# Optimization experiments

Measured on AMD Instinct MI355X. Metric: run time of the kernel, lower is better.

Reference implementation:

```python
import jax, jax.numpy as jnp
import numpy as np

B, NA, NB, E = 2, 256, 256, 512
H1, H2 = 300, 100


def setup_inputs() -> dict:
    key = jax.random.key(0)
    ks = jax.random.split(key, 16)

    def n(k, shape, scale=1.0):
        return jax.random.normal(k, shape, dtype=jnp.float32) * scale

    z = lambda shape: jnp.zeros(shape, jnp.float32)
    return {
        "action_embedding": n(ks[0], (B, E, NA)),
        "anchor_embedding": n(ks[1], (B, E, NB)),
        "action_points": n(ks[2], (B, 3, NA)),
        "anchor_points": n(ks[3], (B, 3, NB)),
        # pairwise MLP kernel params: 2E -> 300 -> 100 -> 1
        "mlp_W1": n(ks[4], (2 * E, H1), (2 * E) ** -0.5),
        "mlp_b1": z((H1,)),
        "mlp_W2": n(ks[5], (H1, H2), H1 ** -0.5),
        "mlp_b2": z((H2,)),
        "mlp_W3": n(ks[6], (H2, 1), H2 ** -0.5),
        "mlp_b3": z((1,)),
        # PointNet [512,64,64,64,128,512] (1x1 convs) + Conv1d(512,1,bias=False)
        "pn_W0": n(ks[7], (64, 512), 512 ** -0.5),
        "pn_b0": z((64,)),
        "pn_W1": n(ks[8], (64, 64), 64 ** -0.5),
        "pn_b1": z((64,)),
        "pn_W2": n(ks[9], (64, 64), 64 ** -0.5),
        "pn_b2": z((64,)),
        "pn_W3": n(ks[10], (128, 64), 64 ** -0.5),
        "pn_b3": z((128,)),
        "pn_W4": n(ks[11], (512, 128), 128 ** -0.5),
        "pn_b4": z((512,)),
        "head_W": n(ks[12], (1, 512), 512 ** -0.5),
    }


def reference(action_embedding, anchor_embedding, action_points, anchor_points,
              mlp_W1, mlp_b1, mlp_W2, mlp_b2, mlp_W3, mlp_b3,
              pn_W0, pn_b0, pn_W1, pn_b1, pn_W2, pn_b2, pn_W3, pn_b3,
              pn_W4, pn_b4, head_W):
    P_A = action_points.transpose(0, 2, 1)      # (B, NA, 3)
    P_B = anchor_points.transpose(0, 2, 1)      # (B, NB, 3)
    Phi_A = action_embedding.transpose(0, 2, 1)  # (B, NA, E)
    Phi_B = anchor_embedding.transpose(0, 2, 1)  # (B, NB, E)
    Ed = Phi_A.shape[-1]

    # --- symmetric pairwise MLP kernel: softplus((mlp(cat(a,b)) + mlp(cat(b,a))) / 2) ---
    # First Linear layer is split so the O(NA*NB*2E) concat is never materialized:
    # cat(a,b) @ W1 == a @ W1[:E] + b @ W1[E:]
    W1a, W1b = mlp_W1[:Ed], mlp_W1[Ed:]

    def mlp_tail(h):  # h: (B, NA, NB, H1) pre-activation of layer 1
        h = jax.nn.relu(h)
        h = jax.nn.relu(h @ mlp_W2 + mlp_b2)
        return (h @ mlp_W3 + mlp_b3)[..., 0]  # (B, NA, NB)

    hA_a = Phi_A @ W1a  # (B, NA, H1)
    hA_b = Phi_A @ W1b
    hB_a = Phi_B @ W1a  # (B, NB, H1)
    hB_b = Phi_B @ W1b
    v1 = mlp_tail(hA_a[:, :, None, :] + hB_b[:, None, :, :] + mlp_b1)  # mlp(cat(x1,x2))
    v2 = mlp_tail(hB_a[:, None, :, :] + hA_b[:, :, None, :] + mlp_b1)  # mlp(cat(x2,x1))
    R_est = jax.nn.softplus((v1 + v2) * 0.5)  # (B, NA, NB) estimated distances

    # --- weighted multilateration (estimate_p), vectorized over (B, NA) ---
    # Linearized LS: ||p||^2 - 2 q_k^T p = r_k^2 - ||q_k||^2; subtract weighted means
    # to eliminate ||p||^2, then solve 3x3 weighted normal equations per action point.
    w = jnp.ones(P_B.shape[:2], R_est.dtype)            # (B, NB) uniform weights (last_attn=False)
    wsum = w.sum(-1, keepdims=True)                      # (B, 1)
    qbar = (w[..., None] * P_B).sum(1) / wsum            # (B, 3)
    bvec = (P_B ** 2).sum(-1)[:, None, :] - R_est ** 2   # (B, NA, NB)
    bbar = (w[:, None, :] * bvec).sum(-1) / wsum         # (B, NA)
    Amat = 2.0 * (P_B - qbar[:, None, :])                # (B, NB, 3)
    yvec = bvec - bbar[..., None]                        # (B, NA, NB)
    M = jnp.einsum('bki,bk,bkj->bij', Amat, w, Amat)     # (B, 3, 3)
    rhs = jnp.einsum('bki,bk,bak->bai', Amat, w, yvec)   # (B, NA, 3)
    P_A_B_pred = jnp.linalg.solve(M[:, None], rhs[..., None])[..., 0]  # (B, NA, 3)

    flow = (P_A_B_pred - P_A).transpose(0, 2, 1)         # (B, 3, NA)

    # --- PointNet flow-weight head (1x1 convs + ReLU, final conv no bias) ---
    x = action_embedding                                  # (B, 512, NA)
    for Wc, bc in ((pn_W0, pn_b0), (pn_W1, pn_b1), (pn_W2, pn_b2),
                   (pn_W3, pn_b3), (pn_W4, pn_b4)):
        x = jax.nn.relu(jnp.einsum('oi,bin->bon', Wc, x) + bc[None, :, None])
    weight = jnp.einsum('oi,bin->bon', head_W, x)        # (B, 1, NA)

    full_flow = jnp.concatenate([flow, weight], axis=1)  # (B, 4, NA)
    return full_flow
```

## Files before the change

### kernel.cpp

```cpp
#include <hip/hip_runtime.h>
#include <hip/hip_bf16.h>
#include <hip/hip_fp16.h>

typedef float f32x4 __attribute__((ext_vector_type(4)));
typedef float f32x16 __attribute__((ext_vector_type(16)));
typedef short s16x8 __attribute__((ext_vector_type(8)));
typedef _Float16 f16x8 __attribute__((ext_vector_type(8)));

#define OFF_EMBT   0u
#define OFF_W1T    1048576u
#define OFF_W2TSW  1662976u
#define OFF_W0BF   1740800u
#define OFF_HA     1806336u
#define OFF_R2     3051520u
#define WS_TOTAL   3575808u

__device__ __forceinline__ int pack_bf2(float a, float b) {
  __hip_bfloat162 h = __float22bfloat162_rn(make_float2(a, b));
  int r; __builtin_memcpy(&r, &h, 4); return r;
}
__device__ __forceinline__ unsigned pack_f16_2(float a, float b) {
  __half2 h = __float22half2_rn(make_float2(a, b));
  unsigned r; __builtin_memcpy(&r, &h, 4); return r;
}
__device__ __forceinline__ unsigned short bf16u(float f) {
  __hip_bfloat16 h = __float2bfloat16(f);
  unsigned short u; __builtin_memcpy(&u, &h, 2); return u;
}
__device__ __forceinline__ s16x8 i4_to_s8(int a, int b, int c, int d) {
  union { int i[4]; s16x8 s; } u;
  u.i[0] = a; u.i[1] = b; u.i[2] = c; u.i[3] = d; return u.s;
}
template<int CTRL>
__device__ __forceinline__ float dpp_add(float x) {
  int xi; __builtin_memcpy(&xi, &x, 4);
  int yi = __builtin_amdgcn_update_dpp(0, xi, CTRL, 0xf, 0xf, true);
  float y; __builtin_memcpy(&y, &yi, 4);
  return x + y;
}
__device__ __forceinline__ float swz_xor16(float x) {
  int xi; __builtin_memcpy(&xi, &x, 4);
  int yi = __builtin_amdgcn_ds_swizzle(xi, 0x401f);
  float y; __builtin_memcpy(&y, &yi, 4);
  return y;
}

__global__ __launch_bounds__(256) void ka_prep(
    const float* __restrict__ act_emb, const float* __restrict__ anc_emb,
    const float* __restrict__ W1, const float* __restrict__ W2,
    const float* __restrict__ W0pn, char* __restrict__ ws)
{
  __hip_bfloat16* embT  = (__hip_bfloat16*)(ws + OFF_EMBT);
  __hip_bfloat16* W1T   = (__hip_bfloat16*)(ws + OFF_W1T);
  unsigned short* W2Tsw = (unsigned short*)(ws + OFF_W2TSW);
  unsigned short* W0bf  = (unsigned short*)(ws + OFF_W0BF);
  __shared__ float tile[64][65];
  int blk = blockIdx.x, t = threadIdx.x;
  if (blk < 128) {
    int b = blk >> 6, emb = (blk >> 5) & 1, ntile = (blk >> 3) & 3, etile = blk & 7;
    const float* src = emb ? anc_emb : act_emb;
    int e0 = etile * 64, n0 = ntile * 64;
    int rr = t >> 6, cc = t & 63;
    #pragma unroll
    for (int it2 = 0; it2 < 16; ++it2) {
      int e_l = rr * 16 + it2;
      tile[e_l][cc] = src[(size_t)(b * 512 + e0 + e_l) * 256 + n0 + cc];
    }
    __syncthreads();
    int n_l = t >> 2, eq = t & 3;
    unsigned int* dst = (unsigned int*)(embT + ((size_t)((b * 2 + emb) * 256 + n0 + n_l)) * 512 + e0 + eq * 16);
    #pragma unroll
    for (int kk = 0; kk < 8; ++kk)
      dst[kk] = (unsigned)pack_bf2(tile[eq * 16 + 2 * kk][n_l], tile[eq * 16 + 2 * kk + 1][n_l]);
  } else if (blk < 208) {
    int id = blk - 128;
    int half = id / 40; int rem = id % 40; int et = rem / 5; int ct = rem % 5;
    int e0 = et * 64, c0 = ct * 64;
    int rr = t >> 6, cc = t & 63;
    #pragma unroll
    for (int it2 = 0; it2 < 16; ++it2) {
      int e_l = rr * 16 + it2;
      int c = c0 + cc;
      tile[e_l][cc] = (c < 300) ? W1[(size_t)(half * 512 + e0 + e_l) * 300 + c] : 0.f;
    }
    __syncthreads();
    int c_l = t >> 2, eq = t & 3;
    if (c0 + c_l < 300) {
      unsigned int* dst = (unsigned int*)(W1T + ((size_t)(half * 300 + c0 + c_l)) * 512 + e0 + eq * 16);
      #pragma unroll
      for (int kk = 0; kk < 8; ++kk)
        dst[kk] = (unsigned)pack_bf2(tile[eq * 16 + 2 * kk][c_l], tile[eq * 16 + 2 * kk + 1][c_l]);
    }
  } else if (blk < 227) {
    int idx = (blk - 208) * 256 + t;
    int lane = idx & 63; int ntks = idx >> 6; int nt = ntks & 3; int ks = ntks >> 2;
    int n = nt * 32 + (lane & 31);
    int kb = ks * 16 + (lane >> 5) * 8;
    unsigned int q[4];
    #pragma unroll
    for (int jj = 0; jj < 4; ++jj) {
      int k0 = kb + jj * 2, k1 = kb + jj * 2 + 1;
      float f0 = (n < 100 && k0 < 300) ? W2[(size_t)k0 * 100 + n] : 0.f;
      float f1 = (n < 100 && k1 < 300) ? W2[(size_t)k1 * 100 + n] : 0.f;
      q[jj] = pack_f16_2(f0, f1);
    }
    ((uint4*)W2Tsw)[idx] = make_uint4(q[0], q[1], q[2], q[3]);
  } else if (blk < 243) {
    int idx = (blk - 227) * 256 + t;
    const float* s = W0pn + (size_t)idx * 8;
    ((uint4*)W0bf)[idx] = make_uint4(
        (unsigned)pack_bf2(s[0], s[1]), (unsigned)pack_bf2(s[2], s[3]),
        (unsigned)pack_bf2(s[4], s[5]), (unsigned)pack_bf2(s[6], s[7]));
  } else {
    int idx = (blk - 243) * 256 + t;
    _Float16* haf = (_Float16*)(ws + OFF_HA);
    #pragma unroll
    for (int u2 = 0; u2 < 2; ++u2) {
      int unit = idx * 2 + u2;
      int combo = unit >> 5, row = unit & 31;
      size_t off = (((size_t)combo * 19 + 18) << 9) + (1 << 8) + (row << 3) + 4;
      unsigned* p = (unsigned*)(haf + off);
      p[0] = 0u; p[1] = 0u;
    }
  }
}

template<int K, int NT>
__device__ __forceinline__ void pn_layer(unsigned short* xb, const float* __restrict__ W,
                                         const float* __restrict__ bias, int wv, int l, int g)
{
  constexpr int NN = NT / 4;
  f32x4 z = {0.f, 0.f, 0.f, 0.f};
  f32x4 acc[NN];
  #pragma unroll
  for (int nn = 0; nn < NN; ++nn) acc[nn] = z;
  #pragma unroll
  for (int nn = 0; nn < NN; ++nn) {
    int o = (wv + nn * 4) * 16 + l;
    const float* wr0 = W + (size_t)o * K;
    #pragma unroll
    for (int ks = 0; ks < K / 32; ++ks) {
      int koff = ks * 32 + g * 8;
      f32x4 wa = *(const f32x4*)(wr0 + koff);
      f32x4 wb = *(const f32x4*)(wr0 + koff + 4);
      s16x8 bfr = i4_to_s8(pack_bf2(wa.x, wa.y), pack_bf2(wa.z, wa.w),
                           pack_bf2(wb.x, wb.y), pack_bf2(wb.z, wb.w));
      s16x8 a0 = *(const s16x8*)(xb + (size_t)l * 520 + koff);
      acc[nn] = __builtin_amdgcn_mfma_f32_16x16x32_bf16(a0, bfr, acc[nn], 0, 0, 0);
    }
  }
  __syncthreads();
  #pragma unroll
  for (int nn = 0; nn < NN; ++nn) {
    int chan = (wv + nn * 4) * 16 + l;
    float bv = bias[chan];
    #pragma unroll
    for (int r = 0; r < 4; ++r)
      xb[(size_t)(g * 4 + r) * 520 + chan] = bf16u(fmaxf(acc[nn][r] + bv, 0.f));
  }
  __syncthreads();
}

__global__ __launch_bounds__(256) void k1_ha(
    const __hip_bfloat16* __restrict__ embT, const __hip_bfloat16* __restrict__ W1T,
    const float* __restrict__ b1, _Float16* __restrict__ ha_f,
    const unsigned short* __restrict__ W0bf,
    const float* __restrict__ pnW1, const float* __restrict__ pnW2,
    const float* __restrict__ pnW3, const float* __restrict__ pnW4,
    const float* __restrict__ pnB0, const float* __restrict__ pnB1,
    const float* __restrict__ pnB2, const float* __restrict__ pnB3,
    const float* __restrict__ pnB4,
    const float* __restrict__ headW, float* __restrict__ out)
{
  __shared__ unsigned short xbuf[16 * 520];
  int blk = blockIdx.x, t = threadIdx.x;
  int wv = t >> 6, lane = t & 63, l = lane & 15, g = lane >> 4;
  if (blk < 320) {
    int b = blk / 160; int r = blk % 160; int emb = r / 80; r %= 80;
    int mch = r / 5; int nch = r % 5;
    int m0 = mch * 16;
    const unsigned short* Ap = (const unsigned short*)embT +
        ((size_t)((b * 2 + emb) * 256 + m0 + l)) * 512;
    const unsigned short* Wp = (const unsigned short*)W1T;
    f32x4 z = {0.f, 0.f, 0.f, 0.f};
    f32x4 acc[2] = {z, z};
    for (int ks = 0; ks < 16; ++ks) {
      int k0 = ks * 32 + g * 8;
      s16x8 af = *(const s16x8*)(Ap + k0);
      #pragma unroll
      for (int q = 0; q < 2; ++q) {
        int c = nch * 120 + (wv * 2 + q) * 16 + l;
        s16x8 bf = {0, 0, 0, 0, 0, 0, 0, 0};
        if (c < 600) bf = *(const s16x8*)(Wp + (size_t)c * 512 + k0);
        acc[q] = __builtin_amdgcn_mfma_f32_16x16x32_bf16(af, bf, acc[q], 0, 0, 0);
      }
    }
    #pragma unroll
    for (int q = 0; q < 2; ++q) {
      int cl = (wv * 2 + q) * 16 + l;
      int c = nch * 120 + cl;
      if (cl < 120 && c < 600) {
        int half = (c >= 300) ? 1 : 0;
        int cc = c - half * 300;
        float bias = (emb == 0) ? b1[cc] : 0.f;
        int d = emb * 2 + half;
        int ksf = cc >> 4, hi2 = (cc >> 3) & 1, e = cc & 7;
        #pragma unroll
        for (int r2 = 0; r2 < 4; ++r2) {
          int i = m0 + g * 4 + r2;
          size_t off = (((((size_t)(b * 4 + d)) * 8 + (i >> 5)) * 19 + ksf) << 9)
                     + (hi2 << 8) + ((i & 31) << 3) + e;
          ha_f[off] = (_Float16)__float2half_rn(acc[q][r2] + bias);
        }
      }
    }
  } else {
    int pn = blk - 320;
    int b_pn = pn >> 4, n0 = (pn & 15) * 16;
    unsigned short* xb = xbuf;
    {
      const unsigned short* A0 = (const unsigned short*)embT + ((size_t)(b_pn * 2 * 256 + n0)) * 512;
      f32x4 acc0 = {0.f, 0.f, 0.f, 0.f};
      int o = wv * 16 + l;
      const unsigned short* w0r = W0bf + (size_t)o * 512;
      #pragma unroll
      for (int ks = 0; ks < 16; ++ks) {
        int koff = ks * 32 + g * 8;
        s16x8 bfr = *(const s16x8*)(w0r + koff);
        s16x8 a0 = *(const s16x8*)(A0 + (size_t)l * 512 + koff);
        acc0 = __builtin_amdgcn_mfma_f32_16x16x32_bf16(a0, bfr, acc0, 0, 0, 0);
      }
      float bv = pnB0[o];
      #pragma unroll
      for (int r2 = 0; r2 < 4; ++r2)
        xb[(size_t)(g * 4 + r2) * 520 + o] = bf16u(fmaxf(acc0[r2] + bv, 0.f));
      __syncthreads();
    }
    pn_layer<64, 4>(xb, pnW1, pnB1, wv, l, g);
    pn_layer<64, 4>(xb, pnW2, pnB2, wv, l, g);
    pn_layer<64, 8>(xb, pnW3, pnB3, wv, l, g);
    pn_layer<128, 32>(xb, pnW4, pnB4, wv, l, g);
    {
      int p_l = t >> 4, os = t & 15;
      const unsigned short* row = xb + (size_t)p_l * 520 + os * 32;
      float s = 0.f;
      #pragma unroll
      for (int c = 0; c < 32; ++c) {
        unsigned int u = ((unsigned int)row[c]) << 16;
        float xv; __builtin_memcpy(&xv, &u, 4);
        s += xv * headW[os * 32 + c];
      }
      s += __shfl_xor(s, 1); s += __shfl_xor(s, 2);
      s += __shfl_xor(s, 4); s += __shfl_xor(s, 8);
      if (os == 0) out[(size_t)(b_pn * 4 + 3) * 256 + n0 + p_l] = s;
    }
  }
}

__global__ __launch_bounds__(512, 2) void k2_main(
    const _Float16* __restrict__ haF, const unsigned short* __restrict__ W2Tsw,
    const float* __restrict__ b2g, const float* __restrict__ W3g, const float* __restrict__ b3g,
    float* __restrict__ R2)
{
  __shared__ int4 w2s[4864];
  int blkp = blockIdx.x, t = threadIdx.x;
  int blk = (blkp & 7) * 64 + (blkp >> 3);
  int wv = t >> 6, lane = t & 63, col = lane & 31, hi = lane >> 5;
  int u = blk; int b = u >> 8; u &= 255; int it = u >> 5; int jtp = u & 31;
  int i0 = it * 32;
  int j = jtp * 8 + wv;
  {
    const int4* w2g = (const int4*)W2Tsw;
    #pragma unroll
    for (int q = 0; q < 9; ++q) { int idx = t + q * 512; w2s[idx] = w2g[idx]; }
    { int idx = t + 9 * 512; if (idx < 4864) w2s[idx] = w2g[idx]; }
  }
  const _Float16* pA0 = haF + ((((size_t)(b * 4 + 0)) * 8 + it) * 19) * 512 + lane * 8;
  const _Float16* pA1 = haF + ((((size_t)(b * 4 + 1)) * 8 + it) * 19) * 512 + lane * 8;
  const _Float16* pB0 = haF + ((((size_t)(b * 4 + 3)) * 8 + (j >> 5)) * 19) * 512
                        + (hi * 32 + (j & 31)) * 8;
  const _Float16* pB1 = haF + ((((size_t)(b * 4 + 2)) * 8 + (j >> 5)) * 19) * 512
                        + (hi * 32 + (j & 31)) * 8;
  f16x8 a0c = *(const f16x8*)(pA0);
  f16x8 a1c = *(const f16x8*)(pA1);
  f16x8 b0c = *(const f16x8*)(pB0);
  f16x8 b1c = *(const f16x8*)(pB1);
  __syncthreads();

  const f16x8 zf = {0, 0, 0, 0, 0, 0, 0, 0};
  f32x16 z16;
  #pragma unroll
  for (int q = 0; q < 16; ++q) z16[q] = 0.f;
  f32x16 acc00 = z16, acc01 = z16, acc02 = z16, acc03 = z16;
  f32x16 acc10 = z16, acc11 = z16, acc12 = z16, acc13 = z16;

  #pragma unroll 1
  for (int ks = 0; ks < 19; ++ks) {
    f16x8 a0n, a1n, b0n, b1n;
    if (ks < 18) {
      int ko = (ks + 1) * 512;
      a0n = *(const f16x8*)(pA0 + ko);
      a1n = *(const f16x8*)(pA1 + ko);
      b0n = *(const f16x8*)(pB0 + ko);
      b1n = *(const f16x8*)(pB1 + ko);
    } else { a0n = a0c; a1n = a1c; b0n = b0c; b1n = b1c; }
    f16x8 af0 = __builtin_elementwise_max(a0c + b0c, zf);
    f16x8 af1 = __builtin_elementwise_max(a1c + b1c, zf);
    const int4* wp = &w2s[ks * 256 + lane];
    f16x8 bf0 = *(const f16x8*)(wp);
    f16x8 bf1 = *(const f16x8*)(wp + 64);
    f16x8 bf2 = *(const f16x8*)(wp + 128);
    f16x8 bf3 = *(const f16x8*)(wp + 192);
    acc00 = __builtin_amdgcn_mfma_f32_32x32x16_f16(af0, bf0, acc00, 0, 0, 0);
    acc10 = __builtin_amdgcn_mfma_f32_32x32x16_f16(af1, bf0, acc10, 0, 0, 0);
    acc01 = __builtin_amdgcn_mfma_f32_32x32x16_f16(af0, bf1, acc01, 0, 0, 0);
    acc11 = __builtin_amdgcn_mfma_f32_32x32x16_f16(af1, bf1, acc11, 0, 0, 0);
    acc02 = __builtin_amdgcn_mfma_f32_32x32x16_f16(af0, bf2, acc02, 0, 0, 0);
    acc12 = __builtin_amdgcn_mfma_f32_32x32x16_f16(af1, bf2, acc12, 0, 0, 0);
    acc03 = __builtin_amdgcn_mfma_f32_32x32x16_f16(af0, bf3, acc03, 0, 0, 0);
    acc13 = __builtin_amdgcn_mfma_f32_32x32x16_f16(af1, bf3, acc13, 0, 0, 0);
    a0c = a0n; a1c = a1n; b0c = b0n; b1c = b1n;
  }
  {
    float w3v[4], b2v[4];
    #pragma unroll
    for (int nt = 0; nt < 4; ++nt) {
      int n = nt * 32 + col;
      w3v[nt] = (n < 100) ? W3g[n] : 0.f;
      b2v[nt] = (n < 100) ? b2g[n] : 0.f;
    }
    float b3 = b3g[0];
    float mine = 0.f;
    #pragma unroll
    for (int r = 0; r < 16; ++r) {
      float x = fmaxf(acc00[r] + b2v[0], 0.f) * w3v[0] + fmaxf(acc10[r] + b2v[0], 0.f) * w3v[0]
              + fmaxf(acc01[r] + b2v[1], 0.f) * w3v[1] + fmaxf(acc11[r] + b2v[1], 0.f) * w3v[1]
              + fmaxf(acc02[r] + b2v[2], 0.f) * w3v[2] + fmaxf(acc12[r] + b2v[2], 0.f) * w3v[2]
              + fmaxf(acc03[r] + b2v[3], 0.f) * w3v[3] + fmaxf(acc13[r] + b2v[3], 0.f) * w3v[3];
      x = dpp_add<0xB1>(x);
      x = dpp_add<0x4E>(x);
      x = dpp_add<0x141>(x);
      x = dpp_add<0x140>(x);
      x += swz_xor16(x);
      if (col == r) mine = x;
    }
    if (col < 16) {
      float S = 0.5f * mine + b3;
      float Rr = (S > 20.f) ? S : log1pf(expf(S));
      int il = (col & 3) + 8 * (col >> 2) + 4 * hi;
      R2[((size_t)(b * 256 + i0 + il)) * 256 + j] = Rr * Rr;
    }
  }
}

__device__ __forceinline__ float block_sum(float v, float* redbuf, int t) {
  #pragma unroll
  for (int m = 1; m < 64; m <<= 1) v += __shfl_xor(v, m);
  __syncthreads();
  if ((t & 63) == 0) redbuf[t >> 6] = v;
  __syncthreads();
  return redbuf[0] + redbuf[1] + redbuf[2] + redbuf[3];
}

__global__ __launch_bounds__(256) void k3_solve(
    const float* __restrict__ anc_pts, const float* __restrict__ act_pts,
    const float* __restrict__ R2, float* __restrict__ out)
{
  __shared__ float Ax[256], Ay[256], Az[256];
  __shared__ float redbuf[4];
  int blk = blockIdx.x, t = threadIdx.x;
  int b = blk >> 2, ic = blk & 3;
  int k = t;
  float px = anc_pts[(size_t)(b * 3 + 0) * 256 + k];
  float py = anc_pts[(size_t)(b * 3 + 1) * 256 + k];
  float pz = anc_pts[(size_t)(b * 3 + 2) * 256 + k];
  float qx = block_sum(px, redbuf, t) * (1.f / 256.f);
  float qy = block_sum(py, redbuf, t) * (1.f / 256.f);
  float qz = block_sum(pz, redbuf, t) * (1.f / 256.f);
  float ax = 2.f * (px - qx), ay = 2.f * (py - qy), az = 2.f * (pz - qz);
  float p2 = px * px + py * py + pz * pz;
  Ax[k] = ax; Ay[k] = ay; Az[k] = az;
  float mxx = block_sum(ax * ax, redbuf, t);
  float mxy = block_sum(ax * ay, redbuf, t);
  float mxz = block_sum(ax * az, redbuf, t);
  float myy = block_sum(ay * ay, redbuf, t);
  float myz = block_sum(ay * az, redbuf, t);
  float mzz = block_sum(az * az, redbuf, t);
  float c0x = block_sum(ax * p2, redbuf, t);
  float c0y = block_sum(ay * p2, redbuf, t);
  float c0z = block_sum(az * p2, redbuf, t);
  __syncthreads();
  float det = mxx * (myy * mzz - myz * myz) - mxy * (mxy * mzz - myz * mxz) + mxz * (mxy * myz - myy * mxz);
  float idet = 1.f / det;
  float i00 = (myy * mzz - myz * myz) * idet;
  float i01 = (mxz * myz - mxy * mzz) * idet;
  float i02 = (mxy * myz - mxz * myy) * idet;
  float i11 = (mxx * mzz - mxz * mxz) * idet;
  float i12 = (mxy * mxz - mxx * myz) * idet;
  float i22 = (mxx * myy - mxy * mxy) * idet;
  int il = t >> 2, ks = t & 3;
  int i = ic * 64 + il;
  const float* rrow = R2 + ((size_t)(b * 256 + i)) * 256;
  float r0 = 0.f, r1 = 0.f, r2 = 0.f;
  #pragma unroll
  for (int kk = 0; kk < 16; ++kk) {
    int kb = ks * 64 + kk * 4;
    f32x4 rv = *(const f32x4*)(rrow + kb);
    r0 += Ax[kb] * rv.x + Ax[kb + 1] * rv.y + Ax[kb + 2] * rv.z + Ax[kb + 3] * rv.w;
    r1 += Ay[kb] * rv.x + Ay[kb + 1] * rv.y + Ay[kb + 2] * rv.z + Ay[kb + 3] * rv.w;
    r2 += Az[kb] * rv.x + Az[kb + 1] * rv.y + Az[kb + 2] * rv.z + Az[kb + 3] * rv.w;
  }
  r0 += __shfl_xor(r0, 1); r0 += __shfl_xor(r0, 2);
  r1 += __shfl_xor(r1, 1); r1 += __shfl_xor(r1, 2);
  r2 += __shfl_xor(r2, 1); r2 += __shfl_xor(r2, 2);
  if (ks == 0) {
    float hx = c0x - r0, hy = c0y - r1, hz = c0z - r2;
    float x0 = i00 * hx + i01 * hy + i02 * hz;
    float x1 = i01 * hx + i11 * hy + i12 * hz;
    float x2 = i02 * hx + i12 * hy + i22 * hz;
    out[(size_t)(b * 4 + 0) * 256 + i] = x0 - act_pts[(size_t)(b * 3 + 0) * 256 + i];
    out[(size_t)(b * 4 + 1) * 256 + i] = x1 - act_pts[(size_t)(b * 3 + 1) * 256 + i];
    out[(size_t)(b * 4 + 2) * 256 + i] = x2 - act_pts[(size_t)(b * 3 + 2) * 256 + i];
  }
}

extern "C" void kernel_launch(void* const* d_in, const int* in_sizes, int n_in,
                              void* d_out, int out_size, void* d_ws, size_t ws_size,
                              hipStream_t stream)
{
  const float* act_emb = (const float*)d_in[0];
  const float* anc_emb = (const float*)d_in[1];
  const float* act_pts = (const float*)d_in[2];
  const float* anc_pts = (const float*)d_in[3];
  const float* W1  = (const float*)d_in[4];
  const float* b1  = (const float*)d_in[5];
  const float* W2  = (const float*)d_in[6];
  const float* b2  = (const float*)d_in[7];
  const float* W3  = (const float*)d_in[8];
  const float* b3  = (const float*)d_in[9];
  const float* pnW0 = (const float*)d_in[10];
  const float* pnB0 = (const float*)d_in[11];
  const float* pnW1 = (const float*)d_in[12];
  const float* pnB1 = (const float*)d_in[13];
  const float* pnW2 = (const float*)d_in[14];
  const float* pnB2 = (const float*)d_in[15];
  const float* pnW3 = (const float*)d_in[16];
  const float* pnB3 = (const float*)d_in[17];
  const float* pnW4 = (const float*)d_in[18];
  const float* pnB4 = (const float*)d_in[19];
  const float* headW = (const float*)d_in[20];
  char* ws = (char*)d_ws;
  __hip_bfloat16* embT  = (__hip_bfloat16*)(ws + OFF_EMBT);
  __hip_bfloat16* W1T   = (__hip_bfloat16*)(ws + OFF_W1T);
  unsigned short* W2Tsw = (unsigned short*)(ws + OFF_W2TSW);
  unsigned short* W0bf  = (unsigned short*)(ws + OFF_W0BF);
  _Float16* ha_f = (_Float16*)(ws + OFF_HA);
  float* R2ws  = (float*)(ws + OFF_R2);
  float* outp  = (float*)d_out;

  ka_prep<<<247, 256, 0, stream>>>(act_emb, anc_emb, W1, W2, pnW0, ws);
  k1_ha<<<352, 256, 0, stream>>>(embT, W1T, b1, ha_f, W0bf,
                                 pnW1, pnW2, pnW3, pnW4, pnB0, pnB1, pnB2, pnB3, pnB4,
                                 headW, outp);
  k2_main<<<512, 512, 0, stream>>>(ha_f, W2Tsw, b2, W3, b3, R2ws);
  k3_solve<<<8, 256, 0, stream>>>(anc_pts, act_pts, R2ws, outp);
}
```

Baseline: 155.2 us.

## Pre-pack PointNet weights to bf16, retile pairwise MLP waves, widen solve grid

PointNet layer weights 1-4 are now converted to bf16 once in the prep kernel, so the per-block fp32 loads and repacking in k1 go away. In k2 each wave now covers two j columns and half of the output-channel tiles instead of one column and all four. This halves the LDS weight-fragment reads per MFMA and loads adjacent B rows together. The two wave halves combine partial sums through a small shared buffer, which adds two barriers. k3_solve launches 16 blocks instead of 8, with each block handling 32 rows, to spread the tail reduction over more CUs.

```diff
diff --git a/kernel.cpp b/kernel.cpp
--- a/kernel.cpp
+++ b/kernel.cpp
@@ -13,7 +13,8 @@
 #define OFF_W0BF   1740800u
 #define OFF_HA     1806336u
 #define OFF_R2     3051520u
-#define WS_TOTAL   3575808u
+#define OFF_PNPK   3575808u
+#define WS_TOTAL   3739648u
 
 __device__ __forceinline__ int pack_bf2(float a, float b) {
   __hip_bfloat162 h = __float22bfloat162_rn(make_float2(a, b));
@@ -26,10 +27,6 @@
 __device__ __forceinline__ unsigned short bf16u(float f) {
   __hip_bfloat16 h = __float2bfloat16(f);
   unsigned short u; __builtin_memcpy(&u, &h, 2); return u;
-}
-__device__ __forceinline__ s16x8 i4_to_s8(int a, int b, int c, int d) {
-  union { int i[4]; s16x8 s; } u;
-  u.i[0] = a; u.i[1] = b; u.i[2] = c; u.i[3] = d; return u.s;
 }
 template<int CTRL>
 __device__ __forceinline__ float dpp_add(float x) {
@@ -48,7 +45,10 @@
 __global__ __launch_bounds__(256) void ka_prep(
     const float* __restrict__ act_emb, const float* __restrict__ anc_emb,
     const float* __restrict__ W1, const float* __restrict__ W2,
-    const float* __restrict__ W0pn, char* __restrict__ ws)
+    const float* __restrict__ W0pn,
+    const float* __restrict__ pnW1, const float* __restrict__ pnW2,
+    const float* __restrict__ pnW3, const float* __restrict__ pnW4,
+    char* __restrict__ ws)
 {
   __hip_bfloat16* embT  = (__hip_bfloat16*)(ws + OFF_EMBT);
   __hip_bfloat16* W1T   = (__hip_bfloat16*)(ws + OFF_W1T);
@@ -111,7 +111,7 @@
     ((uint4*)W0bf)[idx] = make_uint4(
         (unsigned)pack_bf2(s[0], s[1]), (unsigned)pack_bf2(s[2], s[3]),
         (unsigned)pack_bf2(s[4], s[5]), (unsigned)pack_bf2(s[6], s[7]));
-  } else {
+  } else if (blk < 247) {
     int idx = (blk - 243) * 256 + t;
     _Float16* haf = (_Float16*)(ws + OFF_HA);
     #pragma unroll
@@ -122,11 +122,22 @@
       unsigned* p = (unsigned*)(haf + off);
       p[0] = 0u; p[1] = 0u;
     }
+  } else {
+    int idx = (blk - 247) * 256 + t;
+    const float* s;
+    if (idx < 512)       s = pnW1 + (size_t)idx * 8;
+    else if (idx < 1024) s = pnW2 + (size_t)(idx - 512) * 8;
+    else if (idx < 2048) s = pnW3 + (size_t)(idx - 1024) * 8;
+    else                 s = pnW4 + (size_t)(idx - 2048) * 8;
+    unsigned short* pnPK = (unsigned short*)(ws + OFF_PNPK);
+    ((uint4*)pnPK)[idx] = make_uint4(
+        (unsigned)pack_bf2(s[0], s[1]), (unsigned)pack_bf2(s[2], s[3]),
+        (unsigned)pack_bf2(s[4], s[5]), (unsigned)pack_bf2(s[6], s[7]));
   }
 }
 
 template<int K, int NT>
-__device__ __forceinline__ void pn_layer(unsigned short* xb, const float* __restrict__ W,
+__device__ __forceinline__ void pn_layer(unsigned short* xb, const unsigned short* __restrict__ Wp,
                                          const float* __restrict__ bias, int wv, int l, int g)
 {
   constexpr int NN = NT / 4;
@@ -137,14 +148,11 @@
   #pragma unroll
   for (int nn = 0; nn < NN; ++nn) {
     int o = (wv + nn * 4) * 16 + l;
-    const float* wr0 = W + (size_t)o * K;
+    const unsigned short* wr0 = Wp + (size_t)o * K;
     #pragma unroll
     for (int ks = 0; ks < K / 32; ++ks) {
       int koff = ks * 32 + g * 8;
-      f32x4 wa = *(const f32x4*)(wr0 + koff);
-      f32x4 wb = *(const f32x4*)(wr0 + koff + 4);
-      s16x8 bfr = i4_to_s8(pack_bf2(wa.x, wa.y), pack_bf2(wa.z, wa.w),
-                           pack_bf2(wb.x, wb.y), pack_bf2(wb.z, wb.w));
+      s16x8 bfr = *(const s16x8*)(wr0 + koff);
       s16x8 a0 = *(const s16x8*)(xb + (size_t)l * 520 + koff);
       acc[nn] = __builtin_amdgcn_mfma_f32_16x16x32_bf16(a0, bfr, acc[nn], 0, 0, 0);
     }
@@ -164,9 +172,7 @@
 __global__ __launch_bounds__(256) void k1_ha(
     const __hip_bfloat16* __restrict__ embT, const __hip_bfloat16* __restrict__ W1T,
     const float* __restrict__ b1, _Float16* __restrict__ ha_f,
-    const unsigned short* __restrict__ W0bf,
-    const float* __restrict__ pnW1, const float* __restrict__ pnW2,
-    const float* __restrict__ pnW3, const float* __restrict__ pnW4,
+    const unsigned short* __restrict__ W0bf, const unsigned short* __restrict__ pnPK,
     const float* __restrict__ pnB0, const float* __restrict__ pnB1,
     const float* __restrict__ pnB2, const float* __restrict__ pnB3,
     const float* __restrict__ pnB4,
@@ -236,10 +242,10 @@
         xb[(size_t)(g * 4 + r2) * 520 + o] = bf16u(fmaxf(acc0[r2] + bv, 0.f));
       __syncthreads();
     }
-    pn_layer<64, 4>(xb, pnW1, pnB1, wv, l, g);
-    pn_layer<64, 4>(xb, pnW2, pnB2, wv, l, g);
-    pn_layer<64, 8>(xb, pnW3, pnB3, wv, l, g);
-    pn_layer<128, 32>(xb, pnW4, pnB4, wv, l, g);
+    pn_layer<64, 4>(xb, pnPK, pnB1, wv, l, g);
+    pn_layer<64, 4>(xb, pnPK + 4096, pnB2, wv, l, g);
+    pn_layer<64, 8>(xb, pnPK + 8192, pnB3, wv, l, g);
+    pn_layer<128, 32>(xb, pnPK + 16384, pnB4, wv, l, g);
     {
       int p_l = t >> 4, os = t & 15;
       const unsigned short* row = xb + (size_t)p_l * 520 + os * 32;
@@ -263,12 +269,14 @@
     float* __restrict__ R2)
 {
   __shared__ int4 w2s[4864];
+  __shared__ float ex[4][2][2][16];
   int blkp = blockIdx.x, t = threadIdx.x;
   int blk = (blkp & 7) * 64 + (blkp >> 3);
   int wv = t >> 6, lane = t & 63, col = lane & 31, hi = lane >> 5;
+  int jl = wv & 3, nh = wv >> 2;
   int u = blk; int b = u >> 8; u &= 255; int it = u >> 5; int jtp = u & 31;
   int i0 = it * 32;
-  int j = jtp * 8 + wv;
+  int j0 = jtp * 8 + jl * 2;
   {
     const int4* w2g = (const int4*)W2Tsw;
     #pragma unroll
@@ -277,78 +285,91 @@
   }
   const _Float16* pA0 = haF + ((((size_t)(b * 4 + 0)) * 8 + it) * 19) * 512 + lane * 8;
   const _Float16* pA1 = haF + ((((size_t)(b * 4 + 1)) * 8 + it) * 19) * 512 + lane * 8;
-  const _Float16* pB0 = haF + ((((size_t)(b * 4 + 3)) * 8 + (j >> 5)) * 19) * 512
-                        + (hi * 32 + (j & 31)) * 8;
-  const _Float16* pB1 = haF + ((((size_t)(b * 4 + 2)) * 8 + (j >> 5)) * 19) * 512
-                        + (hi * 32 + (j & 31)) * 8;
+  const _Float16* pB00 = haF + ((((size_t)(b * 4 + 3)) * 8 + (j0 >> 5)) * 19) * 512
+                         + (hi * 32 + (j0 & 31)) * 8;
+  const _Float16* pB10 = haF + ((((size_t)(b * 4 + 2)) * 8 + (j0 >> 5)) * 19) * 512
+                         + (hi * 32 + (j0 & 31)) * 8;
   f16x8 a0c = *(const f16x8*)(pA0);
   f16x8 a1c = *(const f16x8*)(pA1);
-  f16x8 b0c = *(const f16x8*)(pB0);
-  f16x8 b1c = *(const f16x8*)(pB1);
+  f16x8 b00c = *(const f16x8*)(pB00);
+  f16x8 b01c = *(const f16x8*)(pB00 + 8);
+  f16x8 b10c = *(const f16x8*)(pB10);
+  f16x8 b11c = *(const f16x8*)(pB10 + 8);
   __syncthreads();
 
   const f16x8 zf = {0, 0, 0, 0, 0, 0, 0, 0};
   f32x16 z16;
   #pragma unroll
   for (int q = 0; q < 16; ++q) z16[q] = 0.f;
-  f32x16 acc00 = z16, acc01 = z16, acc02 = z16, acc03 = z16;
-  f32x16 acc10 = z16, acc11 = z16, acc12 = z16, acc13 = z16;
+  f32x16 aJ0D0N0 = z16, aJ0D0N1 = z16, aJ0D1N0 = z16, aJ0D1N1 = z16;
+  f32x16 aJ1D0N0 = z16, aJ1D0N1 = z16, aJ1D1N0 = z16, aJ1D1N1 = z16;
 
   #pragma unroll 1
   for (int ks = 0; ks < 19; ++ks) {
-    f16x8 a0n, a1n, b0n, b1n;
+    f16x8 a0n, a1n, b00n, b01n, b10n, b11n;
     if (ks < 18) {
       int ko = (ks + 1) * 512;
       a0n = *(const f16x8*)(pA0 + ko);
       a1n = *(const f16x8*)(pA1 + ko);
-      b0n = *(const f16x8*)(pB0 + ko);
-      b1n = *(const f16x8*)(pB1 + ko);
-    } else { a0n = a0c; a1n = a1c; b0n = b0c; b1n = b1c; }
-    f16x8 af0 = __builtin_elementwise_max(a0c + b0c, zf);
-    f16x8 af1 = __builtin_elementwise_max(a1c + b1c, zf);
-    const int4* wp = &w2s[ks * 256 + lane];
-    f16x8 bf0 = *(const f16x8*)(wp);
-    f16x8 bf1 = *(const f16x8*)(wp + 64);
-    f16x8 bf2 = *(const f16x8*)(wp + 128);
-    f16x8 bf3 = *(const f16x8*)(wp + 192);
-    acc00 = __builtin_amdgcn_mfma_f32_32x32x16_f16(af0, bf0, acc00, 0, 0, 0);
-    acc10 = __builtin_amdgcn_mfma_f32_32x32x16_f16(af1, bf0, acc10, 0, 0, 0);
-    acc01 = __builtin_amdgcn_mfma_f32_32x32x16_f16(af0, bf1, acc01, 0, 0, 0);
-    acc11 = __builtin_amdgcn_mfma_f32_32x32x16_f16(af1, bf1, acc11, 0, 0, 0);
-    acc02 = __builtin_amdgcn_mfma_f32_32x32x16_f16(af0, bf2, acc02, 0, 0, 0);
-    acc12 = __builtin_amdgcn_mfma_f32_32x32x16_f16(af1, bf2, acc12, 0, 0, 0);
-    acc03 = __builtin_amdgcn_mfma_f32_32x32x16_f16(af0, bf3, acc03, 0, 0, 0);
-    acc13 = __builtin_amdgcn_mfma_f32_32x32x16_f16(af1, bf3, acc13, 0, 0, 0);
-    a0c = a0n; a1c = a1n; b0c = b0n; b1c = b1n;
+      b00n = *(const f16x8*)(pB00 + ko);
+      b01n = *(const f16x8*)(pB00 + ko + 8);
+      b10n = *(const f16x8*)(pB10 + ko);
+      b11n = *(const f16x8*)(pB10 + ko + 8);
+    } else { a0n = a0c; a1n = a1c; b00n = b00c; b01n = b01c; b10n = b10c; b11n = b11c; }
+    f16x8 af00 = __builtin_elementwise_max(a0c + b00c, zf);
+    f16x8 af01 = __builtin_elementwise_max(a0c + b01c, zf);
+    f16x8 af10 = __builtin_elementwise_max(a1c + b10c, zf);
+    f16x8 af11 = __builtin_elementwise_max(a1c + b11c, zf);
+    const int4* wp = &w2s[ks * 256 + nh * 128 + lane];
+    f16x8 wf0 = *(const f16x8*)(wp);
+    f16x8 wf1 = *(const f16x8*)(wp + 64);
+    aJ0D0N0 = __builtin_amdgcn_mfma_f32_32x32x16_f16(af00, wf0, aJ0D0N0, 0, 0, 0);
+    aJ1D0N0 = __builtin_amdgcn_mfma_f32_32x32x16_f16(af01, wf0, aJ1D0N0, 0, 0, 0);
+    aJ0D1N0 = __builtin_amdgcn_mfma_f32_32x32x16_f16(af10, wf0, aJ0D1N0, 0, 0, 0);
+    aJ1D1N0 = __builtin_amdgcn_mfma_f32_32x32x16_f16(af11, wf0, aJ1D1N0, 0, 0, 0);
+    aJ0D0N1 = __builtin_amdgcn_mfma_f32_32x32x16_f16(af00, wf1, aJ0D0N1, 0, 0, 0);
+    aJ1D0N1 = __builtin_amdgcn_mfma_f32_32x32x16_f16(af01, wf1, aJ1D0N1, 0, 0, 0);
+    aJ0D1N1 = __builtin_amdgcn_mfma_f32_32x32x16_f16(af10, wf1, aJ0D1N1, 0, 0, 0);
+    aJ1D1N1 = __builtin_amdgcn_mfma_f32_32x32x16_f16(af11, wf1, aJ1D1N1, 0, 0, 0);
+    a0c = a0n; a1c = a1n; b00c = b00n; b01c = b01n; b10c = b10n; b11c = b11n;
   }
   {
-    float w3v[4], b2v[4];
-    #pragma unroll
-    for (int nt = 0; nt < 4; ++nt) {
-      int n = nt * 32 + col;
-      w3v[nt] = (n < 100) ? W3g[n] : 0.f;
-      b2v[nt] = (n < 100) ? b2g[n] : 0.f;
+    float w3v[2], b2v[2];
+    #pragma unroll
+    for (int nt2 = 0; nt2 < 2; ++nt2) {
+      int n = (nh * 2 + nt2) * 32 + col;
+      w3v[nt2] = (n < 100) ? W3g[n] : 0.f;
+      b2v[nt2] = (n < 100) ? b2g[n] : 0.f;
     }
     float b3 = b3g[0];
-    float mine = 0.f;
+    float m0 = 0.f, m1 = 0.f;
     #pragma unroll
     for (int r = 0; r < 16; ++r) {
-      float x = fmaxf(acc00[r] + b2v[0], 0.f) * w3v[0] + fmaxf(acc10[r] + b2v[0], 0.f) * w3v[0]
-              + fmaxf(acc01[r] + b2v[1], 0.f) * w3v[1] + fmaxf(acc11[r] + b2v[1], 0.f) * w3v[1]
-              + fmaxf(acc02[r] + b2v[2], 0.f) * w3v[2] + fmaxf(acc12[r] + b2v[2], 0.f) * w3v[2]
-              + fmaxf(acc03[r] + b2v[3], 0.f) * w3v[3] + fmaxf(acc13[r] + b2v[3], 0.f) * w3v[3];
-      x = dpp_add<0xB1>(x);
-      x = dpp_add<0x4E>(x);
-      x = dpp_add<0x141>(x);
-      x = dpp_add<0x140>(x);
-      x += swz_xor16(x);
-      if (col == r) mine = x;
-    }
-    if (col < 16) {
-      float S = 0.5f * mine + b3;
-      float Rr = (S > 20.f) ? S : log1pf(expf(S));
+      float x0 = fmaxf(aJ0D0N0[r] + b2v[0], 0.f) * w3v[0] + fmaxf(aJ0D0N1[r] + b2v[1], 0.f) * w3v[1]
+               + fmaxf(aJ0D1N0[r] + b2v[0], 0.f) * w3v[0] + fmaxf(aJ0D1N1[r] + b2v[1], 0.f) * w3v[1];
+      float x1 = fmaxf(aJ1D0N0[r] + b2v[0], 0.f) * w3v[0] + fmaxf(aJ1D0N1[r] + b2v[1], 0.f) * w3v[1]
+               + fmaxf(aJ1D1N0[r] + b2v[0], 0.f) * w3v[0] + fmaxf(aJ1D1N1[r] + b2v[1], 0.f) * w3v[1];
+      x0 = dpp_add<0xB1>(x0); x1 = dpp_add<0xB1>(x1);
+      x0 = dpp_add<0x4E>(x0); x1 = dpp_add<0x4E>(x1);
+      x0 = dpp_add<0x141>(x0); x1 = dpp_add<0x141>(x1);
+      x0 = dpp_add<0x140>(x0); x1 = dpp_add<0x140>(x1);
+      x0 += swz_xor16(x0); x1 += swz_xor16(x1);
+      if (col == r) { m0 = x0; m1 = x1; }
+    }
+    __syncthreads();
+    if (nh == 1 && col < 16) { ex[jl][0][hi][col] = m0; ex[jl][1][hi][col] = m1; }
+    __syncthreads();
+    if (nh == 0 && col < 16) {
+      float t0 = m0 + ex[jl][0][hi][col];
+      float t1 = m1 + ex[jl][1][hi][col];
+      float S0 = 0.5f * t0 + b3;
+      float S1 = 0.5f * t1 + b3;
+      float R0 = (S0 > 20.f) ? S0 : log1pf(expf(S0));
+      float R1 = (S1 > 20.f) ? S1 : log1pf(expf(S1));
       int il = (col & 3) + 8 * (col >> 2) + 4 * hi;
-      R2[((size_t)(b * 256 + i0 + il)) * 256 + j] = Rr * Rr;
+      float* dst = &R2[((size_t)(b * 256 + i0 + il)) * 256 + j0];
+      dst[0] = R0 * R0;
+      dst[1] = R1 * R1;
     }
   }
 }
@@ -369,7 +390,7 @@
   __shared__ float Ax[256], Ay[256], Az[256];
   __shared__ float redbuf[4];
   int blk = blockIdx.x, t = threadIdx.x;
-  int b = blk >> 2, ic = blk & 3;
+  int b = blk >> 3, ic = blk & 7;
   int k = t;
   float px = anc_pts[(size_t)(b * 3 + 0) * 256 + k];
   float py = anc_pts[(size_t)(b * 3 + 1) * 256 + k];
@@ -398,22 +419,22 @@
   float i11 = (mxx * mzz - mxz * mxz) * idet;
   float i12 = (mxy * mxz - mxx * myz) * idet;
   float i22 = (mxx * myy - mxy * mxy) * idet;
-  int il = t >> 2, ks = t & 3;
-  int i = ic * 64 + il;
+  int il = t >> 3, ksq = t & 7;
+  int i = ic * 32 + il;
   const float* rrow = R2 + ((size_t)(b * 256 + i)) * 256;
   float r0 = 0.f, r1 = 0.f, r2 = 0.f;
   #pragma unroll
-  for (int kk = 0; kk < 16; ++kk) {
-    int kb = ks * 64 + kk * 4;
+  for (int kk = 0; kk < 8; ++kk) {
+    int kb = ksq * 32 + kk * 4;
     f32x4 rv = *(const f32x4*)(rrow + kb);
     r0 += Ax[kb] * rv.x + Ax[kb + 1] * rv.y + Ax[kb + 2] * rv.z + Ax[kb + 3] * rv.w;
     r1 += Ay[kb] * rv.x + Ay[kb + 1] * rv.y + Ay[kb + 2] * rv.z + Ay[kb + 3] * rv.w;
     r2 += Az[kb] * rv.x + Az[kb + 1] * rv.y + Az[kb + 2] * rv.z + Az[kb + 3] * rv.w;
   }
-  r0 += __shfl_xor(r0, 1); r0 += __shfl_xor(r0, 2);
-  r1 += __shfl_xor(r1, 1); r1 += __shfl_xor(r1, 2);
-  r2 += __shfl_xor(r2, 1); r2 += __shfl_xor(r2, 2);
-  if (ks == 0) {
+  r0 += __shfl_xor(r0, 1); r0 += __shfl_xor(r0, 2); r0 += __shfl_xor(r0, 4);
+  r1 += __shfl_xor(r1, 1); r1 += __shfl_xor(r1, 2); r1 += __shfl_xor(r1, 4);
+  r2 += __shfl_xor(r2, 1); r2 += __shfl_xor(r2, 2); r2 += __shfl_xor(r2, 4);
+  if (ksq == 0) {
     float hx = c0x - r0, hy = c0y - r1, hz = c0z - r2;
     float x0 = i00 * hx + i01 * hy + i02 * hz;
     float x1 = i01 * hx + i11 * hy + i12 * hz;
@@ -454,14 +475,16 @@
   __hip_bfloat16* W1T   = (__hip_bfloat16*)(ws + OFF_W1T);
   unsigned short* W2Tsw = (unsigned short*)(ws + OFF_W2TSW);
   unsigned short* W0bf  = (unsigned short*)(ws + OFF_W0BF);
+  unsigned short* pnPK  = (unsigned short*)(ws + OFF_PNPK);
   _Float16* ha_f = (_Float16*)(ws + OFF_HA);
   float* R2ws  = (float*)(ws + OFF_R2);
   float* outp  = (float*)d_out;
 
-  ka_prep<<<247, 256, 0, stream>>>(act_emb, anc_emb, W1, W2, pnW0, ws);
-  k1_ha<<<352, 256, 0, stream>>>(embT, W1T, b1, ha_f, W0bf,
-                                 pnW1, pnW2, pnW3, pnW4, pnB0, pnB1, pnB2, pnB3, pnB4,
+  ka_prep<<<287, 256, 0, stream>>>(act_emb, anc_emb, W1, W2, pnW0,
+                                   pnW1, pnW2, pnW3, pnW4, ws);
+  k1_ha<<<352, 256, 0, stream>>>(embT, W1T, b1, ha_f, W0bf, pnPK,
+                                 pnB0, pnB1, pnB2, pnB3, pnB4,
                                  headW, outp);
   k2_main<<<512, 512, 0, stream>>>(ha_f, W2Tsw, b2, W3, b3, R2ws);
-  k3_solve<<<8, 256, 0, stream>>>(anc_pts, act_pts, R2ws, outp);
-}
+  k3_solve<<<16, 256, 0, stream>>>(anc_pts, act_pts, R2ws, outp);
+}
```

Result: no change. 157.5 us (+1.5%).
